# Optimization experiments

Measured on AMD Instinct MI355X. Metric: run time of the kernel, lower is better.

## Reference

```python
import jax, jax.numpy as jnp
import numpy as np
from jax import lax

DECAY = 0.9
EPS = 1e-12  # F.normalize eps

B, IN_C, H, W_SP = 32, 512, 64, 64
CODE, CLASSES, MEM = 256, 4, 20


def setup_inputs() -> dict:
    key = jax.random.key(0)
    k1, k2, k3, k4, k5 = jax.random.split(key, 5)
    feats = jax.random.normal(k1, (B, IN_C, H, W_SP), dtype=jnp.float32)
    preds = jax.random.uniform(k2, (B, 1, H, W_SP), dtype=jnp.float32)
    labels = jax.random.randint(k3, (B,), 0, CLASSES, dtype=jnp.int64)
    # queue buffer, L2-normalized along code dim as in __init__
    q = jax.random.normal(k4, (CLASSES, MEM, CODE), dtype=jnp.float32)
    queue = q / jnp.maximum(jnp.linalg.norm(q, axis=2, keepdims=True), EPS)
    kw, kb = jax.random.split(k5)
    Wp = jax.random.normal(kw, (CODE, IN_C), dtype=jnp.float32) * (1.0 / np.sqrt(IN_C))
    bp = jax.random.normal(kb, (CODE,), dtype=jnp.float32) * 0.01
    return {"feats": feats, "preds": preds, "labels": labels, "flag": 1,
            "queue": queue, "Wp": Wp, "bp": bp}


def _update_queue(keys, preds, labels, queue):
    # keys: [B, C, H, W] projected feats; preds: [B, 1, H, W]; sequential EMA per sample
    masked = keys * preds                      # broadcast mask
    feat = masked.reshape(keys.shape[0], keys.shape[1], -1).mean(axis=2)  # [B, C]

    def step(q, inp):
        f, l = inp                             # f: [C], l: scalar label
        slot = q[l]                            # [M, C]
        logit = slot @ f                       # [M]  (query @ key)
        upd = logit[:, None] * f[None, :]      # [M, C] (logit @ value.T)
        upd = upd / jnp.maximum(jnp.linalg.norm(upd, axis=1, keepdims=True), EPS)
        q = q.at[l].set(DECAY * slot + (1.0 - DECAY) * upd)
        return q, None

    queue, _ = lax.scan(step, queue, (feat, labels))
    return queue


def reference(feats, preds, labels, flag, queue, Wp, bp):
    # 1x1 conv projection: [B,512,H,W] -> [B,256,H,W]
    x = jnp.einsum('bchw,oc->bohw', feats, Wp) + bp[None, :, None, None]
    if flag == 1:  # 'train' phase: no-grad EMA memory update
        queue = _update_queue(x, preds, labels, queue)
    b, c, h, w = x.shape
    k = x.reshape(b, c, h * w)                 # key = value-key spatial feats [B, C, HW]
    q = queue[labels]                          # per-sample class memory [B, M, C]
    logit = jnp.einsum('bmc,bcn->bmn', q, k)   # [B, M, HW]
    attn = jax.nn.softmax(logit, axis=1)       # softmax over memory slots (dim=0 per sample)
    new_feat = jnp.einsum('bmc,bmn->bcn', q, attn).reshape(b, c, h, w)
    return jnp.concatenate([new_feat, x], axis=1)  # [B, 2C, H, W]
```

## Files before the change

kernel.cpp:

```cpp
#include <hip/hip_runtime.h>

typedef __attribute__((ext_vector_type(4))) float floatx4;
typedef __attribute__((ext_vector_type(8))) short bf16x8;
typedef __attribute__((ext_vector_type(2))) unsigned int uintx2;
typedef __attribute__((ext_vector_type(4))) unsigned int uintx4;

#define HW   4096
#define CIN  512
#define CODE 256
#define MEM  20
#define NCLS 4
#define NB   32

__device__ __forceinline__ unsigned bf16rn(float f) {
    unsigned u = __float_as_uint(f);
    return u + 0x7fffu + ((u >> 16) & 1u);
}

__device__ __forceinline__ int swz(int row, int slot) {
    return slot ^ ((row >> 2) & 3);
}

__global__ __launch_bounds__(256, 2) void gemm_proj_bf16x3(
    const float* __restrict__ feats,
    const float* __restrict__ Wp,
    const float* __restrict__ bp,
    float* __restrict__ out)
{
    __shared__ unsigned short lds[2][4][128][32];

    const int b   = blockIdx.z;
    const int n0  = blockIdx.x * 128;
    const int o0  = blockIdx.y * 128;
    const int tid = threadIdx.x;
    const int lane = tid & 63;
    const int wid  = tid >> 6;
    const int wm = (wid >> 1) * 64;
    const int wn = (wid & 1) * 64;
    const int lr = lane & 15;
    const int lg = lane >> 4;

    const int ar = tid >> 3;
    const int ac = tid & 7;
    const int bn = tid & 127;
    const int bk = (tid >> 7) * 16;

    const float* fb = feats + (size_t)b * CIN * HW + n0 + bn;
    const float* wa = Wp + (size_t)(o0 + ar) * CIN + ac * 4;

    floatx4 acc[4][4];
#pragma unroll
    for (int i = 0; i < 4; ++i)
#pragma unroll
        for (int j = 0; j < 4; ++j)
#pragma unroll
            for (int r = 0; r < 4; ++r) acc[i][j][r] = 0.f;

    floatx4 av[4];
    float   bv[16];

#define G_LOAD(K0)                                                            \
    {                                                                         \
        _Pragma("unroll")                                                     \
        for (int i = 0; i < 4; ++i)                                           \
            av[i] = *(const floatx4*)(wa + (size_t)(32 * i) * CIN + (K0));    \
        _Pragma("unroll")                                                     \
        for (int j = 0; j < 16; ++j)                                          \
            bv[j] = fb[(size_t)((K0) + bk + j) * HW];                         \
    }

#define STAGE(BUF)                                                            \
    {                                                                         \
        _Pragma("unroll")                                                     \
        for (int i = 0; i < 4; ++i) {                                         \
            const int m = ar + 32 * i;                                        \
            unsigned h[4], l[4];                                              \
            _Pragma("unroll")                                                 \
            for (int e = 0; e < 4; ++e) {                                     \
                unsigned r = bf16rn(av[i][e]);                                \
                float hf = __uint_as_float(r & 0xffff0000u);                  \
                h[e] = r;                                                     \
                l[e] = bf16rn(av[i][e] - hf);                                 \
            }                                                                 \
            uintx2 tH, tL;                                                    \
            tH[0] = (h[0] >> 16) | (h[1] & 0xffff0000u);                      \
            tH[1] = (h[2] >> 16) | (h[3] & 0xffff0000u);                      \
            tL[0] = (l[0] >> 16) | (l[1] & 0xffff0000u);                      \
            tL[1] = (l[2] >> 16) | (l[3] & 0xffff0000u);                      \
            const int sA = swz(m, ac >> 1) * 8 + (ac & 1) * 4;                \
            *(uintx2*)&lds[BUF][0][m][sA] = tH;                               \
            *(uintx2*)&lds[BUF][1][m][sA] = tL;                               \
        }                                                                     \
        unsigned ph[8], pl[8];                                                \
        _Pragma("unroll")                                                     \
        for (int p = 0; p < 8; ++p) {                                         \
            unsigned r0 = bf16rn(bv[2 * p]), r1 = bf16rn(bv[2 * p + 1]);      \
            float h0 = __uint_as_float(r0 & 0xffff0000u);                     \
            float h1 = __uint_as_float(r1 & 0xffff0000u);                     \
            unsigned q0 = bf16rn(bv[2 * p] - h0);                             \
            unsigned q1 = bf16rn(bv[2 * p + 1] - h1);                         \
            ph[p] = (r0 >> 16) | (r1 & 0xffff0000u);                          \
            pl[p] = (q0 >> 16) | (q1 & 0xffff0000u);                          \
        }                                                                     \
        const int sb2 = (tid >> 7) * 2;                                       \
        _Pragma("unroll")                                                     \
        for (int u = 0; u < 2; ++u) {                                         \
            const int s = swz(bn, sb2 + u) * 8;                               \
            uintx4 tB, tC;                                                    \
            tB[0] = ph[4 * u];     tB[1] = ph[4 * u + 1];                     \
            tB[2] = ph[4 * u + 2]; tB[3] = ph[4 * u + 3];                     \
            tC[0] = pl[4 * u];     tC[1] = pl[4 * u + 1];                     \
            tC[2] = pl[4 * u + 2]; tC[3] = pl[4 * u + 3];                     \
            *(uintx4*)&lds[BUF][2][bn][s] = tB;                               \
            *(uintx4*)&lds[BUF][3][bn][s] = tC;                               \
        }                                                                     \
    }

#define COMPUTE(BUF)                                                          \
    {                                                                         \
        bf16x8 fah[4], fal[4], fbh[4], fbl[4];                                \
        _Pragma("unroll")                                                     \
        for (int i = 0; i < 4; ++i) {                                         \
            const int rm = wm + i * 16 + lr;                                  \
            const int rn = wn + i * 16 + lr;                                  \
            fah[i] = *(const bf16x8*)&lds[BUF][0][rm][swz(rm, lg) * 8];       \
            fal[i] = *(const bf16x8*)&lds[BUF][1][rm][swz(rm, lg) * 8];       \
            fbh[i] = *(const bf16x8*)&lds[BUF][2][rn][swz(rn, lg) * 8];       \
            fbl[i] = *(const bf16x8*)&lds[BUF][3][rn][swz(rn, lg) * 8];       \
        }                                                                     \
        _Pragma("unroll")                                                     \
        for (int i = 0; i < 4; ++i)                                           \
            _Pragma("unroll")                                                 \
            for (int j = 0; j < 4; ++j) {                                     \
                acc[i][j] = __builtin_amdgcn_mfma_f32_16x16x32_bf16(          \
                    fah[i], fbh[j], acc[i][j], 0, 0, 0);                      \
                acc[i][j] = __builtin_amdgcn_mfma_f32_16x16x32_bf16(          \
                    fah[i], fbl[j], acc[i][j], 0, 0, 0);                      \
                acc[i][j] = __builtin_amdgcn_mfma_f32_16x16x32_bf16(          \
                    fal[i], fbh[j], acc[i][j], 0, 0, 0);                      \
            }                                                                 \
    }

    G_LOAD(0);
    STAGE(0);

#pragma unroll 2
    for (int step = 0; step < 16; ++step) {
        const int cb = step & 1;
        __syncthreads();
        if (step < 15) G_LOAD((step + 1) * 32);
        COMPUTE(cb);
        if (step < 15) STAGE(cb ^ 1);
    }

#undef G_LOAD
#undef STAGE
#undef COMPUTE

#pragma unroll
    for (int i = 0; i < 4; ++i) {
#pragma unroll
        for (int r = 0; r < 4; ++r) {
            const int m = o0 + wm + i * 16 + lg * 4 + r;
            const float bias = bp[m];
            float* orow = out + ((size_t)b * 2 * CODE + CODE + m) * HW
                        + n0 + wn + lr;
#pragma unroll
            for (int j = 0; j < 4; ++j)
                orow[j * 16] = acc[i][j][r] + bias;
        }
    }
}

__global__ __launch_bounds__(256) void featmean_kernel(
    const float* __restrict__ preds,
    const float* __restrict__ out,
    float* __restrict__ featbuf)
{
    const int c0 = blockIdx.x * 16;
    const int b  = blockIdx.y;
    const int tid = threadIdx.x;
    const int w = tid >> 6, lane = tid & 63;

    __shared__ float sp[HW];
    const float* prow = preds + (size_t)b * HW;
#pragma unroll
    for (int j = 0; j < 4; ++j)
        *(floatx4*)&sp[tid * 4 + j * 1024] = *(const floatx4*)(prow + tid * 4 + j * 1024);
    __syncthreads();

    for (int cc = 0; cc < 4; ++cc) {
        const int c = c0 + w * 4 + cc;
        const float* xrow = out + ((size_t)b * 2 * CODE + CODE + c) * HW;
        float s = 0.f;
#pragma unroll 4
        for (int j = 0; j < 16; ++j) {
            floatx4 xv = *(const floatx4*)(xrow + lane * 4 + j * 256);
            floatx4 pv = *(const floatx4*)&sp[lane * 4 + j * 256];
            s += xv[0] * pv[0] + xv[1] * pv[1] + xv[2] * pv[2] + xv[3] * pv[3];
        }
        for (int off = 32; off > 0; off >>= 1) s += __shfl_down(s, off, 64);
        if (lane == 0) featbuf[b * CODE + c] = s * (1.f / HW);
    }
}

__global__ __launch_bounds__(256) void scan_kernel(
    const float* __restrict__ queue_in,
    const float* __restrict__ featbuf,
    const int* __restrict__ labels,
    const int* __restrict__ flag,
    float* __restrict__ qbuf)
{
    const int tid  = threadIdx.x;
    const int w    = tid >> 6;
    const int lane = tid & 63;

    float qreg[MEM][4];
    const float* qr = queue_in + (size_t)w * MEM * CODE;
#pragma unroll
    for (int m = 0; m < MEM; ++m)
#pragma unroll
        for (int j = 0; j < 4; ++j)
            qreg[m][j] = qr[m * CODE + lane + 64 * j];

    if (*flag == 1) {
        for (int b = 0; b < NB; ++b) {
            const int l = labels[b] & 3;
            if (l != w) continue;
            float f[4];
#pragma unroll
            for (int j = 0; j < 4; ++j) f[j] = featbuf[b * CODE + lane + 64 * j];
            float n2 = f[0] * f[0] + f[1] * f[1] + f[2] * f[2] + f[3] * f[3];
#pragma unroll
            for (int off = 1; off < 64; off <<= 1) n2 += __shfl_xor(n2, off, 64);
            const float nrm = sqrtf(n2);
#pragma unroll
            for (int m = 0; m < MEM; ++m) {
                float p = qreg[m][0] * f[0] + qreg[m][1] * f[1]
                        + qreg[m][2] * f[2] + qreg[m][3] * f[3];
#pragma unroll
                for (int off = 1; off < 64; off <<= 1) p += __shfl_xor(p, off, 64);
                const float coef = 0.1f * p / fmaxf(fabsf(p) * nrm, 1e-12f);
#pragma unroll
                for (int j = 0; j < 4; ++j)
                    qreg[m][j] = 0.9f * qreg[m][j] + coef * f[j];
            }
        }
    }

    float* qo = qbuf + (size_t)w * MEM * CODE;
#pragma unroll
    for (int m = 0; m < MEM; ++m)
#pragma unroll
        for (int j = 0; j < 4; ++j)
            qo[m * CODE + lane + 64 * j] = qreg[m][j];
}

__global__ __launch_bounds__(256, 2) void attn_mfma(
    const float* __restrict__ qbuf,
    const int* __restrict__ labels,
    float* __restrict__ out)
{
    __shared__ unsigned short sqh[32][256];
    __shared__ unsigned short sql[32][256];
    __shared__ unsigned short qth[256][40];
    __shared__ unsigned short qtl[256][40];
    __shared__ unsigned short pb[4][16][32];

    const int b    = blockIdx.y;
    const int n0   = blockIdx.x * 256;
    const int tid  = threadIdx.x;
    const int lane = tid & 63;
    const int wid  = tid >> 6;
    const int lidx = lane & 15;
    const int g    = lane >> 4;
    const int l    = labels[b] & 3;

    const float* qsrc = qbuf + (size_t)l * MEM * CODE;
    for (int idx = tid; idx < 32 * 256; idx += 256) {
        const int m = idx >> 8, c = idx & 255;
        const float v = (m < MEM) ? qsrc[m * CODE + c] : 0.f;
        const unsigned rh = bf16rn(v);
        const float hf = __uint_as_float(rh & 0xffff0000u);
        const unsigned rl = bf16rn(v - hf);
        const unsigned short h16 = (unsigned short)(rh >> 16);
        const unsigned short l16 = (unsigned short)(rl >> 16);
        const int cs = (((c >> 3) ^ (m & 7)) << 3) | (c & 7);
        sqh[m][cs] = h16;
        sql[m][cs] = l16;
        qth[c][m] = h16;
        qtl[c][m] = l16;
    }
    __syncthreads();

    const float* xb = out + ((size_t)b * 2 * CODE + CODE) * HW;
    float* ob = out + (size_t)b * 2 * CODE * HW;

    for (int ns = 0; ns < 4; ++ns) {
        const int nb = n0 + wid * 64 + ns * 16;
        const float* xcol = xb + nb + lidx;

        float xr[64];
#pragma unroll
        for (int ks = 0; ks < 8; ++ks)
#pragma unroll
            for (int j = 0; j < 8; ++j)
                xr[ks * 8 + j] = xcol[(size_t)(ks * 32 + g * 8 + j) * HW];

        floatx4 acc0 = {0.f, 0.f, 0.f, 0.f};
        floatx4 acc1 = {0.f, 0.f, 0.f, 0.f};

#pragma unroll
        for (int ks = 0; ks < 8; ++ks) {
            union { uintx4 u; bf16x8 v; } cvh, cvl;
#pragma unroll
            for (int p = 0; p < 4; ++p) {
                const float a0 = xr[ks * 8 + 2 * p];
                const float a1 = xr[ks * 8 + 2 * p + 1];
                const unsigned r0 = bf16rn(a0), r1 = bf16rn(a1);
                const float h0 = __uint_as_float(r0 & 0xffff0000u);
                const float h1 = __uint_as_float(r1 & 0xffff0000u);
                const unsigned q0 = bf16rn(a0 - h0), q1 = bf16rn(a1 - h1);
                cvh.u[p] = (r0 >> 16) | (r1 & 0xffff0000u);
                cvl.u[p] = (q0 >> 16) | (q1 & 0xffff0000u);
            }
            const int s2 = ((ks * 4 + g) ^ (lidx & 7)) * 8;
            const bf16x8 a0h = *(const bf16x8*)&sqh[lidx][s2];
            const bf16x8 a0l = *(const bf16x8*)&sql[lidx][s2];
            const bf16x8 a1h = *(const bf16x8*)&sqh[16 + lidx][s2];
            const bf16x8 a1l = *(const bf16x8*)&sql[16 + lidx][s2];
            acc0 = __builtin_amdgcn_mfma_f32_16x16x32_bf16(a0h, cvh.v, acc0, 0, 0, 0);
            acc0 = __builtin_amdgcn_mfma_f32_16x16x32_bf16(a0h, cvl.v, acc0, 0, 0, 0);
            acc0 = __builtin_amdgcn_mfma_f32_16x16x32_bf16(a0l, cvh.v, acc0, 0, 0, 0);
            acc1 = __builtin_amdgcn_mfma_f32_16x16x32_bf16(a1h, cvh.v, acc1, 0, 0, 0);
            acc1 = __builtin_amdgcn_mfma_f32_16x16x32_bf16(a1h, cvl.v, acc1, 0, 0, 0);
            acc1 = __builtin_amdgcn_mfma_f32_16x16x32_bf16(a1l, cvh.v, acc1, 0, 0, 0);
        }

        float mx = fmaxf(fmaxf(acc0[0], acc0[1]), fmaxf(acc0[2], acc0[3]));
        if (g == 0)
            mx = fmaxf(mx, fmaxf(fmaxf(acc1[0], acc1[1]), fmaxf(acc1[2], acc1[3])));
        mx = fmaxf(mx, __shfl_xor(mx, 16, 64));
        mx = fmaxf(mx, __shfl_xor(mx, 32, 64));

        float e0[4], e1[4], s = 0.f;
#pragma unroll
        for (int r = 0; r < 4; ++r) { e0[r] = __expf(acc0[r] - mx); s += e0[r]; }
#pragma unroll
        for (int r = 0; r < 4; ++r) {
            e1[r] = (g == 0) ? __expf(acc1[r] - mx) : 0.f;
            s += e1[r];
        }
        s += __shfl_xor(s, 16, 64);
        s += __shfl_xor(s, 32, 64);
        const float inv = 1.f / s;

        const unsigned pw0 = (bf16rn(e0[0] * inv) >> 16) | (bf16rn(e0[1] * inv) & 0xffff0000u);
        const unsigned pw1 = (bf16rn(e0[2] * inv) >> 16) | (bf16rn(e0[3] * inv) & 0xffff0000u);
        const unsigned pw2 = (bf16rn(e1[0] * inv) >> 16) | (bf16rn(e1[1] * inv) & 0xffff0000u);
        const unsigned pw3 = (bf16rn(e1[2] * inv) >> 16) | (bf16rn(e1[3] * inv) & 0xffff0000u);
        *(unsigned*)&pb[wid][lidx][g * 4]          = pw0;
        *(unsigned*)&pb[wid][lidx][g * 4 + 2]      = pw1;
        *(unsigned*)&pb[wid][lidx][16 + g * 4]     = pw2;
        *(unsigned*)&pb[wid][lidx][16 + g * 4 + 2] = pw3;

        const bf16x8 pfrag = *(const bf16x8*)&pb[wid][lidx][g * 8];

#pragma unroll
        for (int ct = 0; ct < 16; ++ct) {
            const bf16x8 ath = *(const bf16x8*)&qth[ct * 16 + lidx][g * 8];
            const bf16x8 atl = *(const bf16x8*)&qtl[ct * 16 + lidx][g * 8];
            floatx4 f4 = {0.f, 0.f, 0.f, 0.f};
            f4 = __builtin_amdgcn_mfma_f32_16x16x32_bf16(ath, pfrag, f4, 0, 0, 0);
            f4 = __builtin_amdgcn_mfma_f32_16x16x32_bf16(atl, pfrag, f4, 0, 0, 0);
            float* orow = ob + (size_t)(ct * 16 + g * 4) * HW + nb + lidx;
#pragma unroll
            for (int r = 0; r < 4; ++r) orow[(size_t)r * HW] = f4[r];
        }
    }
}

extern "C" void kernel_launch(void* const* d_in, const int* in_sizes, int n_in,
                              void* d_out, int out_size, void* d_ws, size_t ws_size,
                              hipStream_t stream)
{
    const float* feats  = (const float*)d_in[0];
    const float* preds  = (const float*)d_in[1];
    const int*   labels = (const int*)d_in[2];
    const int*   flag   = (const int*)d_in[3];
    const float* queue  = (const float*)d_in[4];
    const float* Wp     = (const float*)d_in[5];
    const float* bp     = (const float*)d_in[6];
    float* out = (float*)d_out;

    float* featbuf = (float*)d_ws;
    float* qbuf    = featbuf + NB * CODE;

    gemm_proj_bf16x3<<<dim3(HW / 128, CODE / 128, NB), 256, 0, stream>>>(feats, Wp, bp, out);
    featmean_kernel<<<dim3(16, NB), 256, 0, stream>>>(preds, out, featbuf);
    scan_kernel<<<1, 256, 0, stream>>>(queue, featbuf, labels, flag, qbuf);
    attn_mfma<<<dim3(HW / 256, NB), 256, 0, stream>>>(qbuf, labels, out);
}
```

Baseline: 597.7 us.

## Fuse masked feature mean into projection GEMM epilogue and use hardware bf16 pack

```diff
diff --git a/kernel.cpp b/kernel.cpp
--- a/kernel.cpp
+++ b/kernel.cpp
@@ -17,14 +17,38 @@
     return u + 0x7fffu + ((u >> 16) & 1u);
 }
 
+__device__ __forceinline__ unsigned cvt_pk_bf16(float a, float b) {
+    unsigned r;
+    asm("v_cvt_pk_bf16_f32 %0, %1, %2" : "=v"(r) : "v"(a), "v"(b));
+    return r;
+}
+
+struct hl2 { unsigned h, l; };
+
+__device__ __forceinline__ hl2 split2(float a, float b) {
+    hl2 r;
+    r.h = cvt_pk_bf16(a, b);
+    const float ha = __uint_as_float(r.h << 16);
+    const float hb = __uint_as_float(r.h & 0xffff0000u);
+    r.l = cvt_pk_bf16(a - ha, b - hb);
+    return r;
+}
+
 __device__ __forceinline__ int swz(int row, int slot) {
     return slot ^ ((row >> 2) & 3);
+}
+
+__global__ __launch_bounds__(256) void zero_featbuf(float* __restrict__ featbuf)
+{
+    featbuf[blockIdx.x * 256 + threadIdx.x] = 0.f;
 }
 
 __global__ __launch_bounds__(256, 2) void gemm_proj_bf16x3(
     const float* __restrict__ feats,
     const float* __restrict__ Wp,
     const float* __restrict__ bp,
+    const float* __restrict__ preds,
+    float* __restrict__ featbuf,
     float* __restrict__ out)
 {
     __shared__ unsigned short lds[2][4][128][32];
@@ -74,19 +98,11 @@
         _Pragma("unroll")                                                     \
         for (int i = 0; i < 4; ++i) {                                         \
             const int m = ar + 32 * i;                                        \
-            unsigned h[4], l[4];                                              \
-            _Pragma("unroll")                                                 \
-            for (int e = 0; e < 4; ++e) {                                     \
-                unsigned r = bf16rn(av[i][e]);                                \
-                float hf = __uint_as_float(r & 0xffff0000u);                  \
-                h[e] = r;                                                     \
-                l[e] = bf16rn(av[i][e] - hf);                                 \
-            }                                                                 \
+            const hl2 s01 = split2(av[i][0], av[i][1]);                       \
+            const hl2 s23 = split2(av[i][2], av[i][3]);                       \
             uintx2 tH, tL;                                                    \
-            tH[0] = (h[0] >> 16) | (h[1] & 0xffff0000u);                      \
-            tH[1] = (h[2] >> 16) | (h[3] & 0xffff0000u);                      \
-            tL[0] = (l[0] >> 16) | (l[1] & 0xffff0000u);                      \
-            tL[1] = (l[2] >> 16) | (l[3] & 0xffff0000u);                      \
+            tH[0] = s01.h; tH[1] = s23.h;                                     \
+            tL[0] = s01.l; tL[1] = s23.l;                                     \
             const int sA = swz(m, ac >> 1) * 8 + (ac & 1) * 4;                \
             *(uintx2*)&lds[BUF][0][m][sA] = tH;                               \
             *(uintx2*)&lds[BUF][1][m][sA] = tL;                               \
@@ -94,13 +110,8 @@
         unsigned ph[8], pl[8];                                                \
         _Pragma("unroll")                                                     \
         for (int p = 0; p < 8; ++p) {                                         \
-            unsigned r0 = bf16rn(bv[2 * p]), r1 = bf16rn(bv[2 * p + 1]);      \
-            float h0 = __uint_as_float(r0 & 0xffff0000u);                     \
-            float h1 = __uint_as_float(r1 & 0xffff0000u);                     \
-            unsigned q0 = bf16rn(bv[2 * p] - h0);                             \
-            unsigned q1 = bf16rn(bv[2 * p + 1] - h1);                         \
-            ph[p] = (r0 >> 16) | (r1 & 0xffff0000u);                          \
-            pl[p] = (q0 >> 16) | (q1 & 0xffff0000u);                          \
+            const hl2 sp = split2(bv[2 * p], bv[2 * p + 1]);                  \
+            ph[p] = sp.h; pl[p] = sp.l;                                       \
         }                                                                     \
         const int sb2 = (tid >> 7) * 2;                                       \
         _Pragma("unroll")                                                     \
@@ -157,6 +168,11 @@
 #undef STAGE
 #undef COMPUTE
 
+    float pv[4];
+#pragma unroll
+    for (int j = 0; j < 4; ++j)
+        pv[j] = preds[(size_t)b * HW + n0 + wn + j * 16 + lr];
+
 #pragma unroll
     for (int i = 0; i < 4; ++i) {
 #pragma unroll
@@ -165,42 +181,20 @@
             const float bias = bp[m];
             float* orow = out + ((size_t)b * 2 * CODE + CODE + m) * HW
                         + n0 + wn + lr;
-#pragma unroll
-            for (int j = 0; j < 4; ++j)
-                orow[j * 16] = acc[i][j][r] + bias;
-        }
-    }
-}
-
-__global__ __launch_bounds__(256) void featmean_kernel(
-    const float* __restrict__ preds,
-    const float* __restrict__ out,
-    float* __restrict__ featbuf)
-{
-    const int c0 = blockIdx.x * 16;
-    const int b  = blockIdx.y;
-    const int tid = threadIdx.x;
-    const int w = tid >> 6, lane = tid & 63;
-
-    __shared__ float sp[HW];
-    const float* prow = preds + (size_t)b * HW;
-#pragma unroll
-    for (int j = 0; j < 4; ++j)
-        *(floatx4*)&sp[tid * 4 + j * 1024] = *(const floatx4*)(prow + tid * 4 + j * 1024);
-    __syncthreads();
-
-    for (int cc = 0; cc < 4; ++cc) {
-        const int c = c0 + w * 4 + cc;
-        const float* xrow = out + ((size_t)b * 2 * CODE + CODE + c) * HW;
-        float s = 0.f;
-#pragma unroll 4
-        for (int j = 0; j < 16; ++j) {
-            floatx4 xv = *(const floatx4*)(xrow + lane * 4 + j * 256);
-            floatx4 pv = *(const floatx4*)&sp[lane * 4 + j * 256];
-            s += xv[0] * pv[0] + xv[1] * pv[1] + xv[2] * pv[2] + xv[3] * pv[3];
-        }
-        for (int off = 32; off > 0; off >>= 1) s += __shfl_down(s, off, 64);
-        if (lane == 0) featbuf[b * CODE + c] = s * (1.f / HW);
+            float part = 0.f;
+#pragma unroll
+            for (int j = 0; j < 4; ++j) {
+                const float xv = acc[i][j][r] + bias;
+                orow[j * 16] = xv;
+                part += xv * pv[j];
+            }
+            part += __shfl_xor(part, 1, 64);
+            part += __shfl_xor(part, 2, 64);
+            part += __shfl_xor(part, 4, 64);
+            part += __shfl_xor(part, 8, 64);
+            if (lr == 0)
+                atomicAdd(&featbuf[b * CODE + m], part * (1.f / HW));
+        }
     }
 }
 
@@ -315,14 +309,9 @@
             union { uintx4 u; bf16x8 v; } cvh, cvl;
 #pragma unroll
             for (int p = 0; p < 4; ++p) {
-                const float a0 = xr[ks * 8 + 2 * p];
-                const float a1 = xr[ks * 8 + 2 * p + 1];
-                const unsigned r0 = bf16rn(a0), r1 = bf16rn(a1);
-                const float h0 = __uint_as_float(r0 & 0xffff0000u);
-                const float h1 = __uint_as_float(r1 & 0xffff0000u);
-                const unsigned q0 = bf16rn(a0 - h0), q1 = bf16rn(a1 - h1);
-                cvh.u[p] = (r0 >> 16) | (r1 & 0xffff0000u);
-                cvl.u[p] = (q0 >> 16) | (q1 & 0xffff0000u);
+                const hl2 sp = split2(xr[ks * 8 + 2 * p], xr[ks * 8 + 2 * p + 1]);
+                cvh.u[p] = sp.h;
+                cvl.u[p] = sp.l;
             }
             const int s2 = ((ks * 4 + g) ^ (lidx & 7)) * 8;
             const bf16x8 a0h = *(const bf16x8*)&sqh[lidx][s2];
@@ -355,10 +344,10 @@
         s += __shfl_xor(s, 32, 64);
         const float inv = 1.f / s;
 
-        const unsigned pw0 = (bf16rn(e0[0] * inv) >> 16) | (bf16rn(e0[1] * inv) & 0xffff0000u);
-        const unsigned pw1 = (bf16rn(e0[2] * inv) >> 16) | (bf16rn(e0[3] * inv) & 0xffff0000u);
-        const unsigned pw2 = (bf16rn(e1[0] * inv) >> 16) | (bf16rn(e1[1] * inv) & 0xffff0000u);
-        const unsigned pw3 = (bf16rn(e1[2] * inv) >> 16) | (bf16rn(e1[3] * inv) & 0xffff0000u);
+        const unsigned pw0 = cvt_pk_bf16(e0[0] * inv, e0[1] * inv);
+        const unsigned pw1 = cvt_pk_bf16(e0[2] * inv, e0[3] * inv);
+        const unsigned pw2 = cvt_pk_bf16(e1[0] * inv, e1[1] * inv);
+        const unsigned pw3 = cvt_pk_bf16(e1[2] * inv, e1[3] * inv);
         *(unsigned*)&pb[wid][lidx][g * 4]          = pw0;
         *(unsigned*)&pb[wid][lidx][g * 4 + 2]      = pw1;
         *(unsigned*)&pb[wid][lidx][16 + g * 4]     = pw2;
@@ -396,8 +385,9 @@
     float* featbuf = (float*)d_ws;
     float* qbuf    = featbuf + NB * CODE;
 
-    gemm_proj_bf16x3<<<dim3(HW / 128, CODE / 128, NB), 256, 0, stream>>>(feats, Wp, bp, out);
-    featmean_kernel<<<dim3(16, NB), 256, 0, stream>>>(preds, out, featbuf);
+    zero_featbuf<<<dim3(NB), 256, 0, stream>>>(featbuf);
+    gemm_proj_bf16x3<<<dim3(HW / 128, CODE / 128, NB), 256, 0, stream>>>(
+        feats, Wp, bp, preds, featbuf, out);
     scan_kernel<<<1, 256, 0, stream>>>(queue, featbuf, labels, flag, qbuf);
     attn_mfma<<<dim3(HW / 256, NB), 256, 0, stream>>>(qbuf, labels, out);
 }
```

Measured after the change: 595.2 us. About the same (-0.4%).
